# Kernel tuning notes

Hardware: AMD Instinct MI355X
Metric: run time of the kernel (lower is better)

## Reference

```python
import jax, jax.numpy as jnp
import numpy as np

D_MODEL = 512
N_HEADS = 8
HEAD_DIM = 64
INNER = N_HEADS * HEAD_DIM
PAD = 128  # flash-attention style tile padding used by the custom kernel


def setup_inputs() -> dict:
    key = jax.random.key(0)
    ks = jax.random.split(key, 5)
    B, S = 2, 2048
    scale = 0.02
    return {
        "hidden_states": jax.random.normal(ks[0], (B, S, D_MODEL), dtype=jnp.float32),
        "Wq": jax.random.normal(ks[1], (D_MODEL, INNER), dtype=jnp.float32) * scale,
        "Wk": jax.random.normal(ks[2], (D_MODEL, INNER), dtype=jnp.float32) * scale,
        "Wv": jax.random.normal(ks[3], (D_MODEL, INNER), dtype=jnp.float32) * scale,
        "Wo": jax.random.normal(ks[4], (INNER, D_MODEL), dtype=jnp.float32) * scale,
    }


def _padded_attention(q, k, v):
    """Emulates torch.ops.knl.fwd: pad seq to a multiple of PAD, run
    non-causal scaled dot-product attention masking padded keys, then
    slice back to the original length. q,k,v: [B, S, INNER]."""
    B, S, _ = q.shape
    pad_len = (-S) % PAD
    Sp = S + pad_len
    pad_cfg = ((0, 0), (0, pad_len), (0, 0))
    qp = jnp.pad(q, pad_cfg)
    kp = jnp.pad(k, pad_cfg)
    vp = jnp.pad(v, pad_cfg)
    # [B, H, Sp, hd]
    qh = qp.reshape(B, Sp, N_HEADS, HEAD_DIM).transpose(0, 2, 1, 3)
    kh = kp.reshape(B, Sp, N_HEADS, HEAD_DIM).transpose(0, 2, 1, 3)
    vh = vp.reshape(B, Sp, N_HEADS, HEAD_DIM).transpose(0, 2, 1, 3)
    scale = 1.0 / np.sqrt(HEAD_DIM).astype(np.float32)
    scores = jnp.einsum("bhqd,bhkd->bhqk", qh, kh) * scale  # [B,H,Sp,Sp]
    key_valid = jnp.arange(Sp) < S  # mask out padded keys
    scores = jnp.where(key_valid[None, None, None, :], scores, jnp.float32(-1e30))
    probs = jax.nn.softmax(scores, axis=-1)
    out = jnp.einsum("bhqk,bhkd->bhqd", probs, vh)  # [B,H,Sp,hd]
    out = out.transpose(0, 2, 1, 3).reshape(B, Sp, INNER)
    return out[:, :S, :]


def reference(hidden_states, Wq, Wk, Wv, Wo):
    q = hidden_states @ Wq
    k = hidden_states @ Wk
    v = hidden_states @ Wv
    attn = _padded_attention(q, k, v)
    return attn @ Wo
```

## Files before the change

kernel.cpp:

```cpp
#include <hip/hip_runtime.h>

using bf16 = __bf16;
using bf16x4 = __attribute__((ext_vector_type(4))) __bf16;
using bf16x8 = __attribute__((ext_vector_type(8))) __bf16;
using floatx4 = __attribute__((ext_vector_type(4))) float;
using half4 = __attribute__((ext_vector_type(4))) _Float16;
using half8 = __attribute__((ext_vector_type(8))) _Float16;

#define D_MODEL 512
#define S_LEN 2048
#define HD 64
#define NH 8
#define M_TOT 4096
#define NSPLIT 4
#define KSPAN (S_LEN / NSPLIT)
#define QSCALE 0.18033688f

__device__ __forceinline__ bf16x8 ld8(const bf16* p) {
    return *reinterpret_cast<const bf16x8*>(p);
}
__device__ __forceinline__ void gl_lds16(const bf16* g, bf16* l) {
    __builtin_amdgcn_global_load_lds(
        (const __attribute__((address_space(1))) void*)g,
        (__attribute__((address_space(3))) void*)l, 16, 0, 0);
}

__global__ __launch_bounds__(256) void prep(const float* __restrict__ w0,
                                            const float* __restrict__ w1,
                                            const float* __restrict__ w2,
                                            const float* __restrict__ w3,
                                            const float* __restrict__ X,
                                            bf16* __restrict__ WT,
                                            bf16* __restrict__ Xb) {
    int z = blockIdx.z;
    if (z == 4) {
        int i = (blockIdx.x * 256 + threadIdx.x) * 8;
        float4 a = *reinterpret_cast<const float4*>(X + i);
        float4 b = *reinterpret_cast<const float4*>(X + i + 4);
        bf16x8 o;
        o[0] = (bf16)a.x; o[1] = (bf16)a.y; o[2] = (bf16)a.z; o[3] = (bf16)a.w;
        o[4] = (bf16)b.x; o[5] = (bf16)b.y; o[6] = (bf16)b.z; o[7] = (bf16)b.w;
        *reinterpret_cast<bf16x8*>(Xb + i) = o;
        return;
    }
    if (blockIdx.x >= 256) return;
    __shared__ float t[32][33];
    const float* in = z == 0 ? w0 : z == 1 ? w1 : z == 2 ? w2 : w3;
    bf16* o = WT + (size_t)z * D_MODEL * D_MODEL;
    int x = threadIdx.x & 31;
    int y = threadIdx.x >> 5;
    int k0 = (blockIdx.x & 15) * 32, n0 = (blockIdx.x >> 4) * 32;
    for (int r = y; r < 32; r += 8) t[r][x] = in[(size_t)(k0 + r) * D_MODEL + n0 + x];
    __syncthreads();
    for (int r = y; r < 32; r += 8) o[(size_t)(n0 + r) * D_MODEL + k0 + x] = (bf16)t[x][r];
}

__global__ __launch_bounds__(256) void gemm_qkvf(const bf16* __restrict__ X,
                                                 const bf16* __restrict__ WT,
                                                 bf16* __restrict__ qk,
                                                 bf16* __restrict__ VT) {
    __shared__ __align__(16) bf16 As[64 * 64];
    __shared__ __align__(16) bf16 Bs[64 * 64];
    int lane = threadIdx.x & 63, wave = threadIdx.x >> 6;
    int l15 = lane & 15, quad = lane >> 4;
    int m0 = blockIdx.x * 64;
    int n0 = blockIdx.y * 64;
    int z = n0 >> 9;
    int h = (n0 >> 6) & 7;
    int wm = (wave & 1) * 32, wn = (wave >> 1) * 32;
    float oscale = (z == 0) ? QSCALE : 1.0f;

    int sr = lane >> 3;
    int sc = (lane & 7) ^ sr;
    const bf16* gA = X  + (size_t)(m0 + wave * 16 + sr) * D_MODEL + sc * 8;
    const bf16* gB = WT + (size_t)(n0 + wave * 16 + sr) * D_MODEL + sc * 8;
    bf16* ldsA = &As[(wave * 16) * 64];
    bf16* ldsB = &Bs[(wave * 16) * 64];
    int rx = l15 & 7;

    floatx4 acc[2][2] = {};
    for (int k0 = 0; k0 < D_MODEL; k0 += 64) {
        __syncthreads();
        gl_lds16(gA + k0, ldsA);
        gl_lds16(gA + (size_t)8 * D_MODEL + k0, ldsA + 8 * 64);
        gl_lds16(gB + k0, ldsB);
        gl_lds16(gB + (size_t)8 * D_MODEL + k0, ldsB + 8 * 64);
        __syncthreads();
        bf16x8 af[2][2], bfr[2][2];
        #pragma unroll
        for (int mt = 0; mt < 2; mt++)
            #pragma unroll
            for (int kh = 0; kh < 2; kh++)
                af[mt][kh] = ld8(&As[(wm + mt * 16 + l15) * 64 + (((quad + 4 * kh) ^ rx)) * 8]);
        #pragma unroll
        for (int nt = 0; nt < 2; nt++)
            #pragma unroll
            for (int kh = 0; kh < 2; kh++)
                bfr[nt][kh] = ld8(&Bs[(wn + nt * 16 + l15) * 64 + (((quad + 4 * kh) ^ rx)) * 8]);
        #pragma unroll
        for (int mt = 0; mt < 2; mt++)
            #pragma unroll
            for (int nt = 0; nt < 2; nt++) {
                acc[mt][nt] = __builtin_amdgcn_mfma_f32_16x16x32_bf16(af[mt][0], bfr[nt][0], acc[mt][nt], 0, 0, 0);
                acc[mt][nt] = __builtin_amdgcn_mfma_f32_16x16x32_bf16(af[mt][1], bfr[nt][1], acc[mt][nt], 0, 0, 0);
            }
    }

    if (z < 2) {
        bf16* dst = qk + (size_t)z * M_TOT * HD * NH;
        #pragma unroll
        for (int mt = 0; mt < 2; mt++)
            #pragma unroll
            for (int nt = 0; nt < 2; nt++)
                #pragma unroll
                for (int r = 0; r < 4; r++) {
                    int m = m0 + wm + mt * 16 + quad * 4 + r;
                    int n = wn + nt * 16 + l15;
                    int b = m >> 11, s = m & 2047;
                    dst[((size_t)(b * NH + h) * S_LEN + s) * HD + n] = (bf16)(acc[mt][nt][r] * oscale);
                }
    } else {
        #pragma unroll
        for (int mt = 0; mt < 2; mt++)
            #pragma unroll
            for (int nt = 0; nt < 2; nt++) {
                int m = m0 + wm + mt * 16 + quad * 4;
                int d = wn + nt * 16 + l15;
                int b = m >> 11, s = m & 2047;
                bf16x4 pk;
                pk[0] = (bf16)acc[mt][nt][0]; pk[1] = (bf16)acc[mt][nt][1];
                pk[2] = (bf16)acc[mt][nt][2]; pk[3] = (bf16)acc[mt][nt][3];
                *reinterpret_cast<bf16x4*>(&VT[((size_t)(b * NH + h) * HD + d) * S_LEN + s]) = pk;
            }
    }
}

__global__ __launch_bounds__(256, 4) void attn_split(const bf16* __restrict__ qg,
                                                     const bf16* __restrict__ kg,
                                                     const bf16* __restrict__ vt,
                                                     _Float16* __restrict__ Opart,
                                                     float* __restrict__ lsum) {
    __shared__ __align__(16) bf16 Kl[64 * 64];
    __shared__ __align__(16) bf16 Vl[64 * 64];
    int tid = threadIdx.x;
    int lane = tid & 63, wave = tid >> 6;
    int l15 = lane & 15, quad = lane >> 4;
    int bh = blockIdx.y, split = blockIdx.z;
    int q0 = blockIdx.x * 128;
    const bf16* qb = qg + (size_t)bh * S_LEN * HD;
    const bf16* kb = kg + (size_t)bh * S_LEN * HD + (size_t)split * KSPAN * HD;
    const bf16* vb = vt + (size_t)bh * HD * S_LEN + split * KSPAN;
    int qA = q0 + wave * 32 + l15;
    int qB = qA + 16;
    bf16x8 qf[2][2];
    qf[0][0] = ld8(qb + (size_t)qA * HD + quad * 8);
    qf[0][1] = ld8(qb + (size_t)qA * HD + 32 + quad * 8);
    qf[1][0] = ld8(qb + (size_t)qB * HD + quad * 8);
    qf[1][1] = ld8(qb + (size_t)qB * HD + 32 + quad * 8);
    floatx4 O[2][4] = {};
    float l_i[2] = {0.f, 0.f};

    int sr = lane >> 3;
    int sc = (lane & 7) ^ sr;
    const bf16* gK = kb + (size_t)(wave * 16 + sr) * HD + sc * 8;
    const bf16* gV = vb + (size_t)(wave * 16 + sr) * S_LEN + sc * 8;
    bf16* ldsK = &Kl[(wave * 16) * 64];
    bf16* ldsV = &Vl[(wave * 16) * 64];
    int rx = l15 & 7;
    int sa = ((quad & 1) << 5) + l15;
    int sb = sa + 16;
    bool himux = (quad & 2) != 0;

    for (int kt = 0; kt < KSPAN; kt += 64) {
        __syncthreads();
        gl_lds16(gK + (size_t)kt * HD, ldsK);
        gl_lds16(gK + (size_t)(kt + 8) * HD, ldsK + 8 * 64);
        gl_lds16(gV + kt, ldsV);
        gl_lds16(gV + (size_t)8 * S_LEN + kt, ldsV + 8 * 64);
        __syncthreads();

        floatx4 sc4[2][4];
        #pragma unroll
        for (int nt = 0; nt < 4; nt++) {
            bf16x8 a0 = ld8(&Kl[(nt * 16 + l15) * 64 + (quad ^ rx) * 8]);
            bf16x8 a1 = ld8(&Kl[(nt * 16 + l15) * 64 + ((quad + 4) ^ rx) * 8]);
            #pragma unroll
            for (int s = 0; s < 2; s++) {
                floatx4 z = {};
                z = __builtin_amdgcn_mfma_f32_16x16x32_bf16(a0, qf[s][0], z, 0, 0, 0);
                z = __builtin_amdgcn_mfma_f32_16x16x32_bf16(a1, qf[s][1], z, 0, 0, 0);
                sc4[s][nt] = z;
            }
        }

        bf16x8 pb[2][2];
        #pragma unroll
        for (int s = 0; s < 2; s++) {
            int2 pq[4];
            #pragma unroll
            for (int nt = 0; nt < 4; nt++) {
                bf16x4 pk;
                #pragma unroll
                for (int r = 0; r < 4; r++) {
                    float p = exp2f(sc4[s][nt][r]);
                    l_i[s] += p;
                    pk[r] = (bf16)p;
                }
                pq[nt] = __builtin_bit_cast(int2, pk);
            }
            #pragma unroll
            for (int h2 = 0; h2 < 2; h2++) {
                int t0 = __shfl(pq[2 * h2].x,     sa, 64);
                int t1 = __shfl(pq[2 * h2].y,     sa, 64);
                int t2 = __shfl(pq[2 * h2 + 1].x, sa, 64);
                int t3 = __shfl(pq[2 * h2 + 1].y, sa, 64);
                int u0 = __shfl(pq[2 * h2].x,     sb, 64);
                int u1 = __shfl(pq[2 * h2].y,     sb, 64);
                int u2 = __shfl(pq[2 * h2 + 1].x, sb, 64);
                int u3 = __shfl(pq[2 * h2 + 1].y, sb, 64);
                int4 v;
                v.x = himux ? t2 : t0;
                v.y = himux ? t3 : t1;
                v.z = himux ? u2 : u0;
                v.w = himux ? u3 : u1;
                pb[s][h2] = __builtin_bit_cast(bf16x8, v);
            }
        }

        #pragma unroll
        for (int nt = 0; nt < 4; nt++) {
            bf16x8 v0 = ld8(&Vl[(nt * 16 + l15) * 64 + (quad ^ rx) * 8]);
            bf16x8 v1 = ld8(&Vl[(nt * 16 + l15) * 64 + ((quad + 4) ^ rx) * 8]);
            #pragma unroll
            for (int s = 0; s < 2; s++) {
                O[s][nt] = __builtin_amdgcn_mfma_f32_16x16x32_bf16(v0, pb[s][0], O[s][nt], 0, 0, 0);
                O[s][nt] = __builtin_amdgcn_mfma_f32_16x16x32_bf16(v1, pb[s][1], O[s][nt], 0, 0, 0);
            }
        }
    }

    #pragma unroll
    for (int s = 0; s < 2; s++) {
        l_i[s] += __shfl_xor(l_i[s], 16, 64);
        l_i[s] += __shfl_xor(l_i[s], 32, 64);
        int q = (s == 0) ? qA : qB;
        size_t obase = (((size_t)(split * 16 + bh)) * S_LEN + q) * HD;
        #pragma unroll
        for (int nt = 0; nt < 4; nt++) {
            half4 hv;
            hv[0] = (_Float16)O[s][nt][0]; hv[1] = (_Float16)O[s][nt][1];
            hv[2] = (_Float16)O[s][nt][2]; hv[3] = (_Float16)O[s][nt][3];
            *reinterpret_cast<half4*>(&Opart[obase + nt * 16 + quad * 4]) = hv;
        }
        if (quad == 0)
            lsum[((size_t)(split * 16 + bh)) * S_LEN + q] = l_i[s];
    }
}

__global__ __launch_bounds__(256) void gemm_outm(const _Float16* __restrict__ Opart,
                                                 const float* __restrict__ lsum,
                                                 const bf16* __restrict__ WoT,
                                                 float* __restrict__ out) {
    __shared__ __align__(16) bf16 As[64 * 64];
    __shared__ __align__(16) bf16 Bs[64 * 64];
    __shared__ float invl[64 * 8];
    int tid = threadIdx.x;
    int lane = tid & 63, wave = tid >> 6;
    int l15 = lane & 15, quad = lane >> 4;
    int m0 = blockIdx.x * 64;
    int n0 = blockIdx.y * 64;
    int wm = (wave & 1) * 32, wn = (wave >> 1) * 32;

    for (int i = tid; i < 512; i += 256) {
        int row = i >> 3, h = i & 7;
        int mm = m0 + row;
        int b = mm >> 11, q = mm & 2047;
        float l = 0.f;
        #pragma unroll
        for (int s = 0; s < NSPLIT; s++)
            l += lsum[((size_t)(s * 16 + b * NH + h)) * S_LEN + q];
        invl[i] = 1.f / l;
    }

    int sr = lane >> 3;
    int sc = (lane & 7) ^ sr;
    const bf16* gB = WoT + (size_t)(n0 + wave * 16 + sr) * D_MODEL + sc * 8;
    bf16* ldsA = &As[(wave * 16) * 64];
    bf16* ldsB = &Bs[(wave * 16) * 64];
    int rx = l15 & 7;

    floatx4 acc[2][2] = {};
    for (int k0 = 0; k0 < D_MODEL; k0 += 64) {
        __syncthreads();
        gl_lds16(gB + k0, ldsB);
        gl_lds16(gB + (size_t)8 * D_MODEL + k0, ldsB + 8 * 64);
        int h = k0 >> 6;
        #pragma unroll
        for (int st = 0; st < 2; st++) {
            int row = wave * 16 + sr + st * 8;
            int mm = m0 + row;
            int b = mm >> 11, q = mm & 2047;
            float iv = invl[row * 8 + h];
            float a8[8] = {};
            #pragma unroll
            for (int s = 0; s < NSPLIT; s++) {
                half8 hp = *reinterpret_cast<const half8*>(
                    &Opart[(((size_t)(s * 16 + b * NH + h)) * S_LEN + q) * HD + sc * 8]);
                #pragma unroll
                for (int j = 0; j < 8; j++) a8[j] += (float)hp[j];
            }
            bf16x8 v;
            #pragma unroll
            for (int j = 0; j < 8; j++) v[j] = (bf16)(a8[j] * iv);
            *reinterpret_cast<bf16x8*>(ldsA + st * 512 + lane * 8) = v;
        }
        __syncthreads();
        bf16x8 af[2][2], bfr[2][2];
        #pragma unroll
        for (int mt = 0; mt < 2; mt++)
            #pragma unroll
            for (int kh = 0; kh < 2; kh++)
                af[mt][kh] = ld8(&As[(wm + mt * 16 + l15) * 64 + (((quad + 4 * kh) ^ rx)) * 8]);
        #pragma unroll
        for (int nt = 0; nt < 2; nt++)
            #pragma unroll
            for (int kh = 0; kh < 2; kh++)
                bfr[nt][kh] = ld8(&Bs[(wn + nt * 16 + l15) * 64 + (((quad + 4 * kh) ^ rx)) * 8]);
        #pragma unroll
        for (int mt = 0; mt < 2; mt++)
            #pragma unroll
            for (int nt = 0; nt < 2; nt++) {
                acc[mt][nt] = __builtin_amdgcn_mfma_f32_16x16x32_bf16(af[mt][0], bfr[nt][0], acc[mt][nt], 0, 0, 0);
                acc[mt][nt] = __builtin_amdgcn_mfma_f32_16x16x32_bf16(af[mt][1], bfr[nt][1], acc[mt][nt], 0, 0, 0);
            }
    }

    #pragma unroll
    for (int mt = 0; mt < 2; mt++)
        #pragma unroll
        for (int nt = 0; nt < 2; nt++)
            #pragma unroll
            for (int r = 0; r < 4; r++) {
                int m = m0 + wm + mt * 16 + quad * 4 + r;
                int n = n0 + wn + nt * 16 + l15;
                out[(size_t)m * D_MODEL + n] = acc[mt][nt][r];
            }
}

extern "C" void kernel_launch(void* const* d_in, const int* in_sizes, int n_in,
                              void* d_out, int out_size, void* d_ws, size_t ws_size,
                              hipStream_t stream) {
    const float* X  = (const float*)d_in[0];
    const float* Wq = (const float*)d_in[1];
    const float* Wk = (const float*)d_in[2];
    const float* Wv = (const float*)d_in[3];
    const float* Wo = (const float*)d_in[4];
    float* out = (float*)d_out;
    bf16* ws  = (bf16*)d_ws;

    bf16* Xb  = ws;
    bf16* WT  = Xb + (size_t)M_TOT * D_MODEL;
    bf16* qk  = WT + (size_t)4 * D_MODEL * D_MODEL;
    bf16* VT  = qk + (size_t)2 * M_TOT * D_MODEL;
    _Float16* Opart = (_Float16*)(VT + (size_t)M_TOT * D_MODEL);
    float* lbuf = (float*)(Opart + (size_t)NSPLIT * 16 * S_LEN * HD);

    prep<<<dim3(1024, 1, 5), 256, 0, stream>>>(Wq, Wk, Wv, Wo, X, WT, Xb);
    gemm_qkvf<<<dim3(64, 24), 256, 0, stream>>>(Xb, WT, qk, VT);
    attn_split<<<dim3(16, 16, NSPLIT), 256, 0, stream>>>(qk,
                                                         qk + (size_t)M_TOT * D_MODEL,
                                                         VT, Opart, lbuf);
    gemm_outm<<<dim3(64, 8), 256, 0, stream>>>(Opart, lbuf,
                                               WT + (size_t)3 * D_MODEL * D_MODEL, out);
}
```

Before: 132.6 us.

## Double-buffer LDS tiles in QKV GEMM and split attention kernels

Both the QKV projection GEMM and the split-K attention kernel now keep two LDS buffers. Each iteration issues the async global-to-LDS loads for the next tile before computing on the current one, and uses one barrier per iteration instead of two. The goal is to hide global load latency behind MFMA work. LDS use per block doubles, which may cut occupancy for the attention kernel launched with 4 blocks per CU. The barrier also relies on the async LDS loads having completed before the tile is read.

```diff
diff --git a/kernel.cpp b/kernel.cpp
--- a/kernel.cpp
+++ b/kernel.cpp
@@ -59,8 +59,8 @@
                                                  const bf16* __restrict__ WT,
                                                  bf16* __restrict__ qk,
                                                  bf16* __restrict__ VT) {
-    __shared__ __align__(16) bf16 As[64 * 64];
-    __shared__ __align__(16) bf16 Bs[64 * 64];
+    __shared__ __align__(16) bf16 As[2][64 * 64];
+    __shared__ __align__(16) bf16 Bs[2][64 * 64];
     int lane = threadIdx.x & 63, wave = threadIdx.x >> 6;
     int l15 = lane & 15, quad = lane >> 4;
     int m0 = blockIdx.x * 64;
@@ -74,29 +74,35 @@
     int sc = (lane & 7) ^ sr;
     const bf16* gA = X  + (size_t)(m0 + wave * 16 + sr) * D_MODEL + sc * 8;
     const bf16* gB = WT + (size_t)(n0 + wave * 16 + sr) * D_MODEL + sc * 8;
-    bf16* ldsA = &As[(wave * 16) * 64];
-    bf16* ldsB = &Bs[(wave * 16) * 64];
+    int ldsOff = (wave * 16) * 64;
     int rx = l15 & 7;
 
+    gl_lds16(gA, &As[0][ldsOff]);
+    gl_lds16(gA + (size_t)8 * D_MODEL, &As[0][ldsOff + 8 * 64]);
+    gl_lds16(gB, &Bs[0][ldsOff]);
+    gl_lds16(gB + (size_t)8 * D_MODEL, &Bs[0][ldsOff + 8 * 64]);
+    __syncthreads();
+
     floatx4 acc[2][2] = {};
+    int cur = 0;
     for (int k0 = 0; k0 < D_MODEL; k0 += 64) {
-        __syncthreads();
-        gl_lds16(gA + k0, ldsA);
-        gl_lds16(gA + (size_t)8 * D_MODEL + k0, ldsA + 8 * 64);
-        gl_lds16(gB + k0, ldsB);
-        gl_lds16(gB + (size_t)8 * D_MODEL + k0, ldsB + 8 * 64);
-        __syncthreads();
+        if (k0 + 64 < D_MODEL) {
+            gl_lds16(gA + k0 + 64, &As[cur ^ 1][ldsOff]);
+            gl_lds16(gA + (size_t)8 * D_MODEL + k0 + 64, &As[cur ^ 1][ldsOff + 8 * 64]);
+            gl_lds16(gB + k0 + 64, &Bs[cur ^ 1][ldsOff]);
+            gl_lds16(gB + (size_t)8 * D_MODEL + k0 + 64, &Bs[cur ^ 1][ldsOff + 8 * 64]);
+        }
         bf16x8 af[2][2], bfr[2][2];
         #pragma unroll
         for (int mt = 0; mt < 2; mt++)
             #pragma unroll
             for (int kh = 0; kh < 2; kh++)
-                af[mt][kh] = ld8(&As[(wm + mt * 16 + l15) * 64 + (((quad + 4 * kh) ^ rx)) * 8]);
+                af[mt][kh] = ld8(&As[cur][(wm + mt * 16 + l15) * 64 + (((quad + 4 * kh) ^ rx)) * 8]);
         #pragma unroll
         for (int nt = 0; nt < 2; nt++)
             #pragma unroll
             for (int kh = 0; kh < 2; kh++)
-                bfr[nt][kh] = ld8(&Bs[(wn + nt * 16 + l15) * 64 + (((quad + 4 * kh) ^ rx)) * 8]);
+                bfr[nt][kh] = ld8(&Bs[cur][(wn + nt * 16 + l15) * 64 + (((quad + 4 * kh) ^ rx)) * 8]);
         #pragma unroll
         for (int mt = 0; mt < 2; mt++)
             #pragma unroll
@@ -104,6 +110,8 @@
                 acc[mt][nt] = __builtin_amdgcn_mfma_f32_16x16x32_bf16(af[mt][0], bfr[nt][0], acc[mt][nt], 0, 0, 0);
                 acc[mt][nt] = __builtin_amdgcn_mfma_f32_16x16x32_bf16(af[mt][1], bfr[nt][1], acc[mt][nt], 0, 0, 0);
             }
+        __syncthreads();
+        cur ^= 1;
     }
 
     if (z < 2) {
@@ -140,8 +148,8 @@
                                                      const bf16* __restrict__ vt,
                                                      _Float16* __restrict__ Opart,
                                                      float* __restrict__ lsum) {
-    __shared__ __align__(16) bf16 Kl[64 * 64];
-    __shared__ __align__(16) bf16 Vl[64 * 64];
+    __shared__ __align__(16) bf16 Kl[2][64 * 64];
+    __shared__ __align__(16) bf16 Vl[2][64 * 64];
     int tid = threadIdx.x;
     int lane = tid & 63, wave = tid >> 6;
     int l15 = lane & 15, quad = lane >> 4;
@@ -164,26 +172,32 @@
     int sc = (lane & 7) ^ sr;
     const bf16* gK = kb + (size_t)(wave * 16 + sr) * HD + sc * 8;
     const bf16* gV = vb + (size_t)(wave * 16 + sr) * S_LEN + sc * 8;
-    bf16* ldsK = &Kl[(wave * 16) * 64];
-    bf16* ldsV = &Vl[(wave * 16) * 64];
+    int ldsOff = (wave * 16) * 64;
     int rx = l15 & 7;
     int sa = ((quad & 1) << 5) + l15;
     int sb = sa + 16;
     bool himux = (quad & 2) != 0;
 
+    gl_lds16(gK, &Kl[0][ldsOff]);
+    gl_lds16(gK + (size_t)8 * HD, &Kl[0][ldsOff + 8 * 64]);
+    gl_lds16(gV, &Vl[0][ldsOff]);
+    gl_lds16(gV + (size_t)8 * S_LEN, &Vl[0][ldsOff + 8 * 64]);
+    __syncthreads();
+
+    int cur = 0;
     for (int kt = 0; kt < KSPAN; kt += 64) {
-        __syncthreads();
-        gl_lds16(gK + (size_t)kt * HD, ldsK);
-        gl_lds16(gK + (size_t)(kt + 8) * HD, ldsK + 8 * 64);
-        gl_lds16(gV + kt, ldsV);
-        gl_lds16(gV + (size_t)8 * S_LEN + kt, ldsV + 8 * 64);
-        __syncthreads();
+        if (kt + 64 < KSPAN) {
+            gl_lds16(gK + (size_t)(kt + 64) * HD, &Kl[cur ^ 1][ldsOff]);
+            gl_lds16(gK + (size_t)(kt + 72) * HD, &Kl[cur ^ 1][ldsOff + 8 * 64]);
+            gl_lds16(gV + kt + 64, &Vl[cur ^ 1][ldsOff]);
+            gl_lds16(gV + (size_t)8 * S_LEN + kt + 64, &Vl[cur ^ 1][ldsOff + 8 * 64]);
+        }
 
         floatx4 sc4[2][4];
         #pragma unroll
         for (int nt = 0; nt < 4; nt++) {
-            bf16x8 a0 = ld8(&Kl[(nt * 16 + l15) * 64 + (quad ^ rx) * 8]);
-            bf16x8 a1 = ld8(&Kl[(nt * 16 + l15) * 64 + ((quad + 4) ^ rx) * 8]);
+            bf16x8 a0 = ld8(&Kl[cur][(nt * 16 + l15) * 64 + (quad ^ rx) * 8]);
+            bf16x8 a1 = ld8(&Kl[cur][(nt * 16 + l15) * 64 + ((quad + 4) ^ rx) * 8]);
             #pragma unroll
             for (int s = 0; s < 2; s++) {
                 floatx4 z = {};
@@ -229,14 +243,17 @@
 
         #pragma unroll
         for (int nt = 0; nt < 4; nt++) {
-            bf16x8 v0 = ld8(&Vl[(nt * 16 + l15) * 64 + (quad ^ rx) * 8]);
-            bf16x8 v1 = ld8(&Vl[(nt * 16 + l15) * 64 + ((quad + 4) ^ rx) * 8]);
+            bf16x8 v0 = ld8(&Vl[cur][(nt * 16 + l15) * 64 + (quad ^ rx) * 8]);
+            bf16x8 v1 = ld8(&Vl[cur][(nt * 16 + l15) * 64 + ((quad + 4) ^ rx) * 8]);
             #pragma unroll
             for (int s = 0; s < 2; s++) {
                 O[s][nt] = __builtin_amdgcn_mfma_f32_16x16x32_bf16(v0, pb[s][0], O[s][nt], 0, 0, 0);
                 O[s][nt] = __builtin_amdgcn_mfma_f32_16x16x32_bf16(v1, pb[s][1], O[s][nt], 0, 0, 0);
             }
         }
+
+        __syncthreads();
+        cur ^= 1;
     }
 
     #pragma unroll
```

Result: no change. 133.7 us (+0.8%).
